# Optimization experiments

Measured on AMD Instinct MI355X. Metric: run time of the kernel, lower is better.

The kernel has to match this reference:

```python
import jax, jax.numpy as jnp
import numpy as np

B, S, T = 262144, 16, 12
N_ENZ = 4  # species 0..3 are enzyme forms (E, E2, E3, F)


def _build_mechanism():
    """Deterministic synthetic mechanism: per-transition stoichiometry, enzyme
    gather indices with validity masks, reversibility, and net-effect matrix
    (replicates MechanismODE._build_transition_info)."""
    rng = np.random.default_rng(0)
    from_idx = rng.integers(0, N_ENZ, T).astype(np.int32)
    to_idx = rng.integers(0, N_ENZ, T).astype(np.int32)
    from_valid = np.ones(T, dtype=bool)
    from_valid[rng.choice(T, 2, replace=False)] = False
    to_valid = np.ones(T, dtype=bool)
    to_valid[rng.choice(T, 2, replace=False)] = False
    reversible = rng.random(T) < 0.75
    stoich = np.zeros((T, S), np.float32)
    for i in range(T):
        sub = rng.integers(N_ENZ, S)   # consumed species (coeff -1)
        prod = rng.integers(N_ENZ, S)  # produced species (coeff +1)
        stoich[i, sub] -= 1.0
        if prod != sub:
            stoich[i, prod] += 1.0
    effects = stoich.copy()
    for i in range(T):
        if from_valid[i]:
            effects[i, from_idx[i]] -= 1.0
        if to_valid[i]:
            effects[i, to_idx[i]] += 1.0
    return (jnp.asarray(stoich), jnp.asarray(effects), jnp.asarray(from_idx),
            jnp.asarray(from_valid), jnp.asarray(to_idx), jnp.asarray(to_valid),
            jnp.asarray(reversible))


def setup_inputs() -> dict:
    key = jax.random.key(0)
    k1, k2, k3 = jax.random.split(key, 3)
    stoich, effects, from_idx, from_valid, to_idx, to_valid, reversible = _build_mechanism()
    # concentrations in (0.1, 1.0) -> strictly positive, physically sensible
    y = jax.random.uniform(k1, (B, S), dtype=jnp.float32) * 0.9 + 0.1
    forward_rates = jax.random.uniform(k2, (B, T), dtype=jnp.float32)
    reverse_rates = jax.random.uniform(k3, (B, T), dtype=jnp.float32)
    return {
        "t": jnp.zeros((), jnp.float32),
        "y": y,
        "forward_rates": forward_rates,
        "reverse_rates": reverse_rates,
        "stoich": stoich,
        "effects": effects,
        "from_idx": from_idx,
        "from_valid": from_valid,
        "to_idx": to_idx,
        "to_valid": to_valid,
        "reversible": reversible,
    }


def reference(t, y, forward_rates, reverse_rates, stoich, effects,
              from_idx, from_valid, to_idx, to_valid, reversible):
    # Mass-action exponents: negative stoich coeffs -> substrates (forward),
    # positive coeffs -> products (reverse). Matches the per-transition
    # y[:, idx] ** (-coeff) / ** coeff loops, vectorized over transitions.
    neg_exp = jnp.maximum(-stoich, 0.0)          # [T,S]
    pos_exp = jnp.maximum(stoich, 0.0)           # [T,S]
    yb = y[:, None, :]                           # [B,1,S]
    sub_conc = jnp.prod(yb ** neg_exp[None], axis=-1)   # [B,T]
    prod_conc = jnp.prod(yb ** pos_exp[None], axis=-1)  # [B,T]
    # enzyme gather; ones where the state has no tracked enzyme species
    enz_f = jnp.where(from_valid[None, :], y[:, from_idx], 1.0)  # [B,T]
    enz_r = jnp.where(to_valid[None, :], y[:, to_idx], 1.0)      # [B,T]
    v_fwd = forward_rates * enz_f * sub_conc
    v_rev = jnp.where(reversible[None, :], reverse_rates * enz_r * prod_conc, 0.0)
    v_net = v_fwd - v_rev                        # [B,T]
    # scatter-add of effect * v_net over species == dense contraction with
    # the (sparse) net-effect matrix
    return jnp.einsum("bt,ts->bs", v_net, effects)  # [B,S]
```

## Files before the change

kernel.cpp:

```cpp
#include <hip/hip_runtime.h>

#define S_DIM 16
#define T_DIM 12
#define BLOCK 256
#define YROW  17

__global__ __launch_bounds__(BLOCK) void mech_kernel(
    const float* __restrict__ y,
    const float* __restrict__ fr,
    const float* __restrict__ rr,
    const float* __restrict__ stoich,
    const float* __restrict__ effects,
    const int* __restrict__ from_idx,
    const int* __restrict__ from_valid,
    const int* __restrict__ to_idx,
    const int* __restrict__ to_valid,
    const int* __restrict__ reversible,
    float* __restrict__ out,
    int nb)
{
    __shared__ float s_y[BLOCK * YROW];
    __shared__ float s_eff[T_DIM][S_DIM];
    __shared__ int   s_si[T_DIM], s_fi[T_DIM], s_pi[T_DIM], s_ti[T_DIM];
    __shared__ float s_rg[T_DIM];

    const int tid = threadIdx.x;

    if (tid < T_DIM) {
        int sub = 16, prod = 16;
        #pragma unroll
        for (int s = 0; s < S_DIM; ++s) {
            float v = stoich[tid * S_DIM + s];
            s_eff[tid][s] = effects[tid * S_DIM + s];
            if (v < -0.5f) sub = s;
            if (v >  0.5f) prod = s;
        }
        s_si[tid] = sub;
        s_pi[tid] = prod;
        s_fi[tid] = from_valid[tid] ? from_idx[tid] : 16;
        s_ti[tid] = to_valid[tid]   ? to_idx[tid]   : 16;
        s_rg[tid] = reversible[tid] ? 1.0f : 0.0f;
    }

    const int b  = blockIdx.x * BLOCK + tid;
    const int bc = (b < nb) ? b : 0;

    const float4* yp = (const float4*)(y + (size_t)bc * S_DIM);
    float4 y0 = yp[0], y1 = yp[1], y2 = yp[2], y3 = yp[3];
    float* myY = &s_y[tid * YROW];
    myY[0]  = y0.x; myY[1]  = y0.y; myY[2]  = y0.z; myY[3]  = y0.w;
    myY[4]  = y1.x; myY[5]  = y1.y; myY[6]  = y1.z; myY[7]  = y1.w;
    myY[8]  = y2.x; myY[9]  = y2.y; myY[10] = y2.z; myY[11] = y2.w;
    myY[12] = y3.x; myY[13] = y3.y; myY[14] = y3.z; myY[15] = y3.w;
    myY[16] = 1.0f;
    __syncthreads();

    const float4* fp = (const float4*)(fr + (size_t)bc * T_DIM);
    const float4* rp = (const float4*)(rr + (size_t)bc * T_DIM);
    float4 f0 = fp[0], f1 = fp[1], f2 = fp[2];
    float4 r0 = rp[0], r1 = rp[1], r2 = rp[2];
    const float frv[T_DIM] = {f0.x, f0.y, f0.z, f0.w, f1.x, f1.y, f1.z, f1.w, f2.x, f2.y, f2.z, f2.w};
    const float rrv[T_DIM] = {r0.x, r0.y, r0.z, r0.w, r1.x, r1.y, r1.z, r1.w, r2.x, r2.y, r2.z, r2.w};

    float acc[S_DIM];
    #pragma unroll
    for (int s = 0; s < S_DIM; ++s) acc[s] = 0.0f;

    #pragma unroll
    for (int t = 0; t < T_DIM; ++t) {
        float vf = frv[t] * myY[s_fi[t]] * myY[s_si[t]];
        float vr = s_rg[t] * rrv[t] * myY[s_ti[t]] * myY[s_pi[t]];
        float v  = vf - vr;
        #pragma unroll
        for (int s = 0; s < S_DIM; ++s)
            acc[s] = fmaf(v, s_eff[t][s], acc[s]);
    }

    if (b < nb) {
        float4* op = (float4*)(out + (size_t)bc * S_DIM);
        op[0] = make_float4(acc[0],  acc[1],  acc[2],  acc[3]);
        op[1] = make_float4(acc[4],  acc[5],  acc[6],  acc[7]);
        op[2] = make_float4(acc[8],  acc[9],  acc[10], acc[11]);
        op[3] = make_float4(acc[12], acc[13], acc[14], acc[15]);
    }
}

extern "C" void kernel_launch(void* const* d_in, const int* in_sizes, int n_in,
                              void* d_out, int out_size, void* d_ws, size_t ws_size,
                              hipStream_t stream) {
    const float* y  = (const float*)d_in[1];
    const float* fr = (const float*)d_in[2];
    const float* rr = (const float*)d_in[3];
    const float* st = (const float*)d_in[4];
    const float* ef = (const float*)d_in[5];
    const int* fi = (const int*)d_in[6];
    const int* fv = (const int*)d_in[7];
    const int* ti = (const int*)d_in[8];
    const int* tv = (const int*)d_in[9];
    const int* rv = (const int*)d_in[10];
    float* o = (float*)d_out;

    int nb = in_sizes[1] / S_DIM;
    int grid = (nb + BLOCK - 1) / BLOCK;
    mech_kernel<<<grid, BLOCK, 0, stream>>>(y, fr, rr, st, ef, fi, fv, ti, tv, rv, o, nb);
}
```

Before: 107.5 us.

## Stage y, rates and output through LDS for coalesced global accesses

Each thread used to read its own row of y, fr and rr with strided float4 loads. Now the block loads y, forward rates and reverse rates cooperatively with contiguous float4 accesses into padded shared-memory tiles. The output is staged through shared memory the same way and written back with coalesced float4 stores. The cost is much more LDS use per block (about 43 KB), which may lower occupancy, an extra barrier, and scalar LDS writes that may hit bank conflicts.

```diff
diff --git a/kernel.cpp b/kernel.cpp
--- a/kernel.cpp
+++ b/kernel.cpp
@@ -4,6 +4,7 @@
 #define T_DIM 12
 #define BLOCK 256
 #define YROW  17
+#define RROW  13
 
 __global__ __launch_bounds__(BLOCK) void mech_kernel(
     const float* __restrict__ y,
@@ -19,12 +20,15 @@
     float* __restrict__ out,
     int nb)
 {
-    __shared__ float s_y[BLOCK * YROW];
+    __shared__ float s_y [BLOCK * YROW];
+    __shared__ float s_fr[BLOCK * RROW];
+    __shared__ float s_rr[BLOCK * RROW];
     __shared__ float s_eff[T_DIM][S_DIM];
     __shared__ int   s_si[T_DIM], s_fi[T_DIM], s_pi[T_DIM], s_ti[T_DIM];
     __shared__ float s_rg[T_DIM];
 
     const int tid = threadIdx.x;
+    const size_t row0 = (size_t)blockIdx.x * BLOCK;
 
     if (tid < T_DIM) {
         int sub = 16, prod = 16;
@@ -42,25 +46,44 @@
         s_rg[tid] = reversible[tid] ? 1.0f : 0.0f;
     }
 
-    const int b  = blockIdx.x * BLOCK + tid;
-    const int bc = (b < nb) ? b : 0;
-
-    const float4* yp = (const float4*)(y + (size_t)bc * S_DIM);
-    float4 y0 = yp[0], y1 = yp[1], y2 = yp[2], y3 = yp[3];
-    float* myY = &s_y[tid * YROW];
-    myY[0]  = y0.x; myY[1]  = y0.y; myY[2]  = y0.z; myY[3]  = y0.w;
-    myY[4]  = y1.x; myY[5]  = y1.y; myY[6]  = y1.z; myY[7]  = y1.w;
-    myY[8]  = y2.x; myY[9]  = y2.y; myY[10] = y2.z; myY[11] = y2.w;
-    myY[12] = y3.x; myY[13] = y3.y; myY[14] = y3.z; myY[15] = y3.w;
-    myY[16] = 1.0f;
+    {
+        const float4* gy = (const float4*)y;
+        const size_t base = row0 * 4;
+        const size_t limit = (size_t)nb * 4;
+        #pragma unroll
+        for (int k = 0; k < 4; ++k) {
+            int j = tid + k * BLOCK;
+            size_t jg = base + j;
+            float4 v = (jg < limit) ? gy[jg] : make_float4(0.f, 0.f, 0.f, 0.f);
+            int row = j >> 2, col = (j & 3) << 2;
+            float* p = &s_y[row * YROW + col];
+            p[0] = v.x; p[1] = v.y; p[2] = v.z; p[3] = v.w;
+        }
+        s_y[tid * YROW + 16] = 1.0f;
+    }
+    {
+        const float4* gf = (const float4*)fr;
+        const float4* gr = (const float4*)rr;
+        const size_t base = row0 * 3;
+        const size_t limit = (size_t)nb * 3;
+        #pragma unroll
+        for (int k = 0; k < 3; ++k) {
+            int j = tid + k * BLOCK;
+            size_t jg = base + j;
+            float4 a = make_float4(0.f, 0.f, 0.f, 0.f), c = a;
+            if (jg < limit) { a = gf[jg]; c = gr[jg]; }
+            int row = j / 3, part = j - row * 3;
+            float* pf = &s_fr[row * RROW + part * 4];
+            pf[0] = a.x; pf[1] = a.y; pf[2] = a.z; pf[3] = a.w;
+            float* pr = &s_rr[row * RROW + part * 4];
+            pr[0] = c.x; pr[1] = c.y; pr[2] = c.z; pr[3] = c.w;
+        }
+    }
     __syncthreads();
 
-    const float4* fp = (const float4*)(fr + (size_t)bc * T_DIM);
-    const float4* rp = (const float4*)(rr + (size_t)bc * T_DIM);
-    float4 f0 = fp[0], f1 = fp[1], f2 = fp[2];
-    float4 r0 = rp[0], r1 = rp[1], r2 = rp[2];
-    const float frv[T_DIM] = {f0.x, f0.y, f0.z, f0.w, f1.x, f1.y, f1.z, f1.w, f2.x, f2.y, f2.z, f2.w};
-    const float rrv[T_DIM] = {r0.x, r0.y, r0.z, r0.w, r1.x, r1.y, r1.z, r1.w, r2.x, r2.y, r2.z, r2.w};
+    float* myY = &s_y[tid * YROW];
+    const float* myF = &s_fr[tid * RROW];
+    const float* myR = &s_rr[tid * RROW];
 
     float acc[S_DIM];
     #pragma unroll
@@ -68,20 +91,32 @@
 
     #pragma unroll
     for (int t = 0; t < T_DIM; ++t) {
-        float vf = frv[t] * myY[s_fi[t]] * myY[s_si[t]];
-        float vr = s_rg[t] * rrv[t] * myY[s_ti[t]] * myY[s_pi[t]];
+        float vf = myF[t] * myY[s_fi[t]] * myY[s_si[t]];
+        float vr = s_rg[t] * myR[t] * myY[s_ti[t]] * myY[s_pi[t]];
         float v  = vf - vr;
         #pragma unroll
         for (int s = 0; s < S_DIM; ++s)
             acc[s] = fmaf(v, s_eff[t][s], acc[s]);
     }
 
-    if (b < nb) {
-        float4* op = (float4*)(out + (size_t)bc * S_DIM);
-        op[0] = make_float4(acc[0],  acc[1],  acc[2],  acc[3]);
-        op[1] = make_float4(acc[4],  acc[5],  acc[6],  acc[7]);
-        op[2] = make_float4(acc[8],  acc[9],  acc[10], acc[11]);
-        op[3] = make_float4(acc[12], acc[13], acc[14], acc[15]);
+    #pragma unroll
+    for (int s = 0; s < S_DIM; ++s) myY[s] = acc[s];
+    __syncthreads();
+
+    {
+        float4* go = (float4*)out;
+        const size_t base = row0 * 4;
+        const size_t limit = (size_t)nb * 4;
+        #pragma unroll
+        for (int k = 0; k < 4; ++k) {
+            int j = tid + k * BLOCK;
+            size_t jg = base + j;
+            if (jg < limit) {
+                int row = j >> 2, col = (j & 3) << 2;
+                const float* p = &s_y[row * YROW + col];
+                go[jg] = make_float4(p[0], p[1], p[2], p[3]);
+            }
+        }
     }
 }
 
```

Result: slower. 111.2 us (+3.4%).
